# Kernel tuning notes

Hardware: AMD Instinct MI355X
Metric: run time of the kernel (lower is better)

Reference implementation:

```python
import jax, jax.numpy as jnp
import numpy as np

VOCAB = 32000
D_MODEL = 1024
PATCH_LEN = 16
NHEAD = 8
B = 8
S = 4096


def setup_inputs() -> dict:
    key = jax.random.key(0)
    ks = jax.random.split(key, 8)
    token_inputs = jax.random.randint(ks[0], (B, S), 0, VOCAB, dtype=jnp.int64 if jax.config.jax_enable_x64 else jnp.int32)
    attention_mask = jax.random.randint(ks[1], (B, S), 0, 2).astype(bool)
    emb_weight = jax.random.normal(ks[2], (VOCAB, D_MODEL), dtype=jnp.float32) * 0.02
    patch_query = jax.random.normal(ks[3], (1, 1, D_MODEL), dtype=jnp.float32) * 0.02
    # nn.MultiheadAttention packed in-projection [3D, D] and out projection [D, D]
    lim = 1.0 / np.sqrt(D_MODEL)
    in_proj_w = jax.random.uniform(ks[4], (3 * D_MODEL, D_MODEL), jnp.float32, -lim, lim)
    in_proj_b = jnp.zeros((3 * D_MODEL,), jnp.float32)
    out_w = jax.random.uniform(ks[5], (D_MODEL, D_MODEL), jnp.float32, -lim, lim)
    out_b = jnp.zeros((D_MODEL,), jnp.float32)
    return {
        "token_inputs": token_inputs,
        "attention_mask": attention_mask,
        "emb_weight": emb_weight,
        "patch_query": patch_query,
        "in_proj_w": in_proj_w,
        "in_proj_b": in_proj_b,
        "out_w": out_w,
        "out_b": out_b,
    }


def reference(token_inputs, attention_mask, emb_weight, patch_query, in_proj_w, in_proj_b, out_w, out_b):
    d_model = emb_weight.shape[1]
    h, dh = NHEAD, d_model // NHEAD
    L = PATCH_LEN

    tok_emb = emb_weight[token_inputs]              # [B, S, D]
    bsz, seqlen, _ = tok_emb.shape
    # seqlen chosen divisible by PATCH_LEN -> pad_len == 0 (matches torch path)
    num_patches = seqlen // L
    BP = bsz * num_patches
    patch_tokens = tok_emb.reshape(BP, L, d_model)  # [BP, L, D]
    patch_mask = attention_mask.reshape(BP, L)      # True = valid token

    patch_valid = patch_mask.any(axis=1)            # [BP]
    # force position 0 valid for fully-empty patches (safe softmax)
    safe_mask = patch_mask | ((~patch_valid)[:, None] & (jnp.arange(L) == 0)[None, :])

    wq, wk, wv = jnp.split(in_proj_w, 3, axis=0)    # each [D, D]
    bq, bk, bv = jnp.split(in_proj_b, 3, axis=0)

    q = patch_query[0, 0] @ wq.T + bq               # [D] (same query for all patches)
    k = patch_tokens @ wk.T + bk                    # [BP, L, D]
    v = patch_tokens @ wv.T + bv                    # [BP, L, D]

    qh = q.reshape(h, dh)                           # [H, dh]
    kh = k.reshape(BP, L, h, dh)                    # [BP, L, H, dh]
    vh = v.reshape(BP, L, h, dh)

    scale = 1.0 / jnp.sqrt(jnp.asarray(dh, q.dtype))
    scores = jnp.einsum('hd,blhd->bhl', qh, kh) * scale   # [BP, H, L]
    scores = jnp.where(safe_mask[:, None, :], scores, -jnp.inf)
    attn = jax.nn.softmax(scores, axis=-1)                # [BP, H, L]

    ctx = jnp.einsum('bhl,blhd->bhd', attn, vh).reshape(BP, d_model)
    patch_latent = ctx @ out_w.T + out_b                  # [BP, D]

    patch_latent = patch_latent.reshape(bsz, num_patches, d_model)
    pv = patch_valid.reshape(bsz, num_patches)
    patch_latent = patch_latent * pv[..., None].astype(patch_latent.dtype)
    return patch_latent, pv
```

## Files before the change

kernel.cpp:

```cpp
#include <hip/hip_runtime.h>
#include <stdint.h>

typedef unsigned short u16;

#define OUT_LATENT (2048*1024)
#define SCALE 0.08838834764831845f

typedef float f32x4v __attribute__((ext_vector_type(4)));
typedef short s16x8  __attribute__((ext_vector_type(8)));

static __device__ inline u16 f2bf(float f) {
    union { float f; uint32_t u; } v; v.f = f;
    uint32_t u = v.u;
    return (u16)((u + 0x7FFFu + ((u >> 16) & 1u)) >> 16);
}
static __device__ inline float bflo(uint32_t u) {
    union { uint32_t u; float f; } v; v.u = u << 16; return v.f;
}
static __device__ inline float bfhi(uint32_t u) {
    union { uint32_t u; float f; } v; v.u = u & 0xFFFF0000u; return v.f;
}
static __device__ __forceinline__ void async16(const u16* g, u16* l) {
    __builtin_amdgcn_global_load_lds(
        (const __attribute__((address_space(1))) void*)g,
        (__attribute__((address_space(3))) void*)l, 16, 0, 0);
}

__global__ __launch_bounds__(256) void k_prep(
    const float* __restrict__ ipw, const float* __restrict__ ipb,
    const float* __restrict__ pq, const float* __restrict__ ow,
    u16* __restrict__ wv_dst, u16* __restrict__ ow_dst,
    u16* __restrict__ qkb, float* __restrict__ sb) {
    __shared__ float qs[128];
    __shared__ float part[128];
    int t = threadIdx.x, b = blockIdx.x;

    if (b < 2048) {
        const float* src; u16* dst; int idx;
        if (b < 1024) { src = ipw + (size_t)2048 * 1024; dst = wv_dst; idx = b * 1024 + t * 4; }
        else          { src = ow;                        dst = ow_dst; idx = (b - 1024) * 1024 + t * 4; }
        float4 f = *(const float4*)(src + idx);
        ushort4 o; o.x = f2bf(f.x); o.y = f2bf(f.y); o.z = f2bf(f.z); o.w = f2bf(f.w);
        *(ushort4*)(dst + idx) = o;
        return;
    }

    int bb = b - 2048;
    int h = bb >> 3, jseg = bb & 7;
    {
        int dl = t >> 1, half = t & 1;
        const float* wrow = ipw + (size_t)(h * 128 + dl) * 1024 + half * 512;
        const float* pqh = pq + half * 512;
        float a = 0.f;
        #pragma unroll 8
        for (int j = 0; j < 512; j += 4) {
            float4 w = *(const float4*)(wrow + j);
            float4 p = *(const float4*)(pqh + j);
            a = fmaf(w.x, p.x, a); a = fmaf(w.y, p.y, a);
            a = fmaf(w.z, p.z, a); a = fmaf(w.w, p.w, a);
        }
        a += __shfl_xor(a, 1);
        if (!half) qs[dl] = a + ipb[h * 128 + dl];
    }
    __syncthreads();
    int jl = t & 127, dh = t >> 7;
    float acc = 0.f;
    const float* wbase = ipw + (size_t)(1024 + h * 128 + dh * 64) * 1024 + jseg * 128 + jl;
    #pragma unroll 8
    for (int d = 0; d < 64; ++d)
        acc = fmaf(qs[dh * 64 + d], wbase[(size_t)d * 1024], acc);
    if (dh) part[jl] = acc;
    __syncthreads();
    if (!dh) qkb[h * 1024 + jseg * 128 + jl] = f2bf((acc + part[jl]) * SCALE);
    if (jseg == 0 && t < 64) {
        const float* bk = ipb + 1024 + h * 128;
        float p = qs[t] * bk[t] + qs[t + 64] * bk[t + 64];
        #pragma unroll
        for (int m = 32; m >= 1; m >>= 1) p += __shfl_xor(p, m);
        if (t == 0) sb[h] = p * SCALE;
    }
}

__global__ __launch_bounds__(256) void k_attn(
    const int* __restrict__ tok_ids, const int* __restrict__ amask,
    const float* __restrict__ emb, const u16* __restrict__ qkb,
    const float* __restrict__ sb, u16* __restrict__ Mout,
    float* __restrict__ pv) {
    __shared__ u16 tokL[16][1032];
    __shared__ float scoresP[4][16][8];
    __shared__ float attnL[16][8];
    __shared__ int allzL;

    int bp = blockIdx.x, t = threadIdx.x;
    int wave = t >> 6, lane = t & 63, lrow = lane & 15, quad = lane >> 4;

    if (t < 16) {
        int any = (amask[bp * 16 + t] != 0);
        any |= __shfl_xor(any, 1); any |= __shfl_xor(any, 2);
        any |= __shfl_xor(any, 4); any |= __shfl_xor(any, 8);
        if (t == 0) { pv[bp] = any ? 1.f : 0.f; allzL = any ? 0 : 1; }
    }

    int row = t >> 4, c = t & 15;
    int tid = tok_ids[bp * 16 + row];
    const float* erow = emb + (size_t)tid * 1024;
    float4 ld[8];
    #pragma unroll
    for (int i = 0; i < 8; ++i) ld[i] = *(const float4*)(erow + (c + i * 16) * 4);

    s16x8 bfr[8];
    {
        const u16* qbase = qkb + (lane & 7) * 1024 + wave * 256 + quad * 8;
        #pragma unroll
        for (int s = 0; s < 8; ++s) bfr[s] = *(const s16x8*)(qbase + s * 32);
    }
    #pragma unroll
    for (int i = 0; i < 8; ++i) {
        ushort4 o; o.x = f2bf(ld[i].x); o.y = f2bf(ld[i].y);
        o.z = f2bf(ld[i].z); o.w = f2bf(ld[i].w);
        *(ushort4*)(&tokL[row][(c + i * 16) * 4]) = o;
    }
    #pragma unroll
    for (int i = 0; i < 8; ++i) ld[i] = *(const float4*)(erow + (c + (i + 8) * 16) * 4);
    #pragma unroll
    for (int i = 0; i < 8; ++i) {
        ushort4 o; o.x = f2bf(ld[i].x); o.y = f2bf(ld[i].y);
        o.z = f2bf(ld[i].z); o.w = f2bf(ld[i].w);
        *(ushort4*)(&tokL[row][(c + (i + 8) * 16) * 4]) = o;
    }
    __syncthreads();

    {
        f32x4v acc = (f32x4v){0.f, 0.f, 0.f, 0.f};
        const u16* arow = &tokL[lrow][wave * 256 + quad * 8];
        #pragma unroll
        for (int s = 0; s < 8; ++s) {
            s16x8 af = *(const s16x8*)(arow + s * 32);
            acc = __builtin_amdgcn_mfma_f32_16x16x32_bf16(af, bfr[s], acc, 0, 0, 0);
        }
        if (lrow < 8) {
            #pragma unroll
            for (int r = 0; r < 4; ++r) scoresP[wave][quad * 4 + r][lrow] = acc[r];
        }
    }
    __syncthreads();

    if (t < 128) {
        int hh = t >> 4, ll = t & 15;
        float s = scoresP[0][ll][hh] + scoresP[1][ll][hh]
                + scoresP[2][ll][hh] + scoresP[3][ll][hh] + sb[hh];
        bool valid = (amask[bp * 16 + ll] != 0) || (allzL && ll == 0);
        s = valid ? s : -1e30f;
        float mx = s;
        mx = fmaxf(mx, __shfl_xor(mx, 1)); mx = fmaxf(mx, __shfl_xor(mx, 2));
        mx = fmaxf(mx, __shfl_xor(mx, 4)); mx = fmaxf(mx, __shfl_xor(mx, 8));
        float e = __expf(s - mx);
        float sum = e;
        sum += __shfl_xor(sum, 1); sum += __shfl_xor(sum, 2);
        sum += __shfl_xor(sum, 4); sum += __shfl_xor(sum, 8);
        attnL[ll][hh] = e / sum;
    }
    __syncthreads();

    float macc[8][4];
    #pragma unroll
    for (int h = 0; h < 8; ++h)
        #pragma unroll
        for (int cc = 0; cc < 4; ++cc) macc[h][cc] = 0.f;
    #pragma unroll
    for (int ll = 0; ll < 16; ++ll) {
        uint2 tv = *(const uint2*)(&tokL[ll][t * 4]);
        float t0 = bflo(tv.x), t1 = bfhi(tv.x), t2 = bflo(tv.y), t3 = bfhi(tv.y);
        float4 a0 = *(const float4*)(&attnL[ll][0]);
        float4 a1 = *(const float4*)(&attnL[ll][4]);
        macc[0][0] = fmaf(a0.x, t0, macc[0][0]); macc[0][1] = fmaf(a0.x, t1, macc[0][1]);
        macc[0][2] = fmaf(a0.x, t2, macc[0][2]); macc[0][3] = fmaf(a0.x, t3, macc[0][3]);
        macc[1][0] = fmaf(a0.y, t0, macc[1][0]); macc[1][1] = fmaf(a0.y, t1, macc[1][1]);
        macc[1][2] = fmaf(a0.y, t2, macc[1][2]); macc[1][3] = fmaf(a0.y, t3, macc[1][3]);
        macc[2][0] = fmaf(a0.z, t0, macc[2][0]); macc[2][1] = fmaf(a0.z, t1, macc[2][1]);
        macc[2][2] = fmaf(a0.z, t2, macc[2][2]); macc[2][3] = fmaf(a0.z, t3, macc[2][3]);
        macc[3][0] = fmaf(a0.w, t0, macc[3][0]); macc[3][1] = fmaf(a0.w, t1, macc[3][1]);
        macc[3][2] = fmaf(a0.w, t2, macc[3][2]); macc[3][3] = fmaf(a0.w, t3, macc[3][3]);
        macc[4][0] = fmaf(a1.x, t0, macc[4][0]); macc[4][1] = fmaf(a1.x, t1, macc[4][1]);
        macc[4][2] = fmaf(a1.x, t2, macc[4][2]); macc[4][3] = fmaf(a1.x, t3, macc[4][3]);
        macc[5][0] = fmaf(a1.y, t0, macc[5][0]); macc[5][1] = fmaf(a1.y, t1, macc[5][1]);
        macc[5][2] = fmaf(a1.y, t2, macc[5][2]); macc[5][3] = fmaf(a1.y, t3, macc[5][3]);
        macc[6][0] = fmaf(a1.z, t0, macc[6][0]); macc[6][1] = fmaf(a1.z, t1, macc[6][1]);
        macc[6][2] = fmaf(a1.z, t2, macc[6][2]); macc[6][3] = fmaf(a1.z, t3, macc[6][3]);
        macc[7][0] = fmaf(a1.w, t0, macc[7][0]); macc[7][1] = fmaf(a1.w, t1, macc[7][1]);
        macc[7][2] = fmaf(a1.w, t2, macc[7][2]); macc[7][3] = fmaf(a1.w, t3, macc[7][3]);
    }
    #pragma unroll
    for (int h = 0; h < 8; ++h) {
        ushort4 o;
        o.x = f2bf(macc[h][0]); o.y = f2bf(macc[h][1]);
        o.z = f2bf(macc[h][2]); o.w = f2bf(macc[h][3]);
        *(ushort4*)(Mout + ((size_t)(h * 2048 + bp)) * 1024 + t * 4) = o;
    }
}

__device__ __forceinline__ void gemm128_bk64(
    const u16* __restrict__ A, const u16* __restrict__ B,
    u16* As, u16* Bs, f32x4v acc[4][4]) {
    int t = threadIdx.x;
    int wave = t >> 6, lane = t & 63, lrow = lane & 15, quad = lane >> 4;
    int wm = wave & 1, wn = wave >> 1;
    int tr = t >> 3, tc7 = t & 7;
    #pragma unroll
    for (int mi = 0; mi < 4; ++mi)
        #pragma unroll
        for (int ni = 0; ni < 4; ++ni) acc[mi][ni] = (f32x4v){0.f, 0.f, 0.f, 0.f};
    for (int step = 0; step < 16; ++step) {
        int k0 = step * 64;
        __syncthreads();
        #pragma unroll
        for (int rb = 0; rb < 128; rb += 32) {
            int r = rb + tr;
            int gofs = (tc7 ^ (r & 7)) * 8;
            async16(A + (size_t)r * 1024 + k0 + gofs, As + rb * 64 + t * 8);
            async16(B + (size_t)r * 1024 + k0 + gofs, Bs + rb * 64 + t * 8);
        }
        __syncthreads();
        #pragma unroll
        for (int kk = 0; kk < 2; ++kk) {
            s16x8 af[4], bf[4];
            #pragma unroll
            for (int i = 0; i < 4; ++i) {
                int ra = wm * 64 + i * 16 + lrow;
                af[i] = *(const s16x8*)(As + ra * 64 + (((kk * 4 + quad) ^ (ra & 7)) * 8));
                int rb2 = wn * 64 + i * 16 + lrow;
                bf[i] = *(const s16x8*)(Bs + rb2 * 64 + (((kk * 4 + quad) ^ (rb2 & 7)) * 8));
            }
            #pragma unroll
            for (int mi = 0; mi < 4; ++mi)
                #pragma unroll
                for (int ni = 0; ni < 4; ++ni)
                    acc[mi][ni] = __builtin_amdgcn_mfma_f32_16x16x32_bf16(af[mi], bf[ni], acc[mi][ni], 0, 0, 0);
        }
    }
}

__global__ __launch_bounds__(256) void k_gemm_ctx(
    const u16* __restrict__ M, const u16* __restrict__ wv,
    const float* __restrict__ ipb, u16* __restrict__ ctx) {
    __shared__ u16 As[128 * 64], Bs[128 * 64];
    int mb = blockIdx.x, h = blockIdx.y;
    f32x4v acc[4][4];
    gemm128_bk64(M + ((size_t)h * 2048 + mb * 128) * 1024,
                 wv + (size_t)h * 128 * 1024, As, Bs, acc);
    int t = threadIdx.x, wave = t >> 6, lane = t & 63, lrow = lane & 15, quad = lane >> 4;
    int wm = wave & 1, wn = wave >> 1;
    #pragma unroll
    for (int ni = 0; ni < 4; ++ni) {
        int n_g = h * 128 + wn * 64 + ni * 16 + lrow;
        float bias = ipb[2048 + n_g];
        #pragma unroll
        for (int mi = 0; mi < 4; ++mi) {
            #pragma unroll
            for (int r = 0; r < 4; ++r) {
                int m_g = mb * 128 + wm * 64 + mi * 16 + quad * 4 + r;
                ctx[(size_t)m_g * 1024 + n_g] = f2bf(acc[mi][ni][r] + bias);
            }
        }
    }
}

__global__ __launch_bounds__(256) void k_gemm_out(
    const u16* __restrict__ ctx, const u16* __restrict__ ow,
    const float* __restrict__ outb, const float* __restrict__ pv,
    float* __restrict__ out) {
    __shared__ u16 As[128 * 64], Bs[128 * 64];
    int mb = blockIdx.x, nb = blockIdx.y;
    f32x4v acc[4][4];
    gemm128_bk64(ctx + (size_t)mb * 128 * 1024,
                 ow + (size_t)nb * 128 * 1024, As, Bs, acc);
    int t = threadIdx.x, wave = t >> 6, lane = t & 63, lrow = lane & 15, quad = lane >> 4;
    int wm = wave & 1, wn = wave >> 1;
    #pragma unroll
    for (int ni = 0; ni < 4; ++ni) {
        int n_g = nb * 128 + wn * 64 + ni * 16 + lrow;
        float bias = outb[n_g];
        #pragma unroll
        for (int mi = 0; mi < 4; ++mi) {
            #pragma unroll
            for (int r = 0; r < 4; ++r) {
                int m_g = mb * 128 + wm * 64 + mi * 16 + quad * 4 + r;
                out[(size_t)m_g * 1024 + n_g] = (acc[mi][ni][r] + bias) * pv[m_g];
            }
        }
    }
    if (nb == 0 && t < 128) out[OUT_LATENT + mb * 128 + t] = pv[mb * 128 + t];
}

extern "C" void kernel_launch(void* const* d_in, const int* in_sizes, int n_in,
                              void* d_out, int out_size, void* d_ws, size_t ws_size,
                              hipStream_t stream) {
    const int*   tok = (const int*)d_in[0];
    const int*   msk = (const int*)d_in[1];
    const float* emb = (const float*)d_in[2];
    const float* pq  = (const float*)d_in[3];
    const float* ipw = (const float*)d_in[4];
    const float* ipb = (const float*)d_in[5];
    const float* ow  = (const float*)d_in[6];
    const float* ob  = (const float*)d_in[7];
    float* out = (float*)d_out;
    char* ws = (char*)d_ws;

    float* sb_f  = (float*)(ws + 4096);
    float* pv_f  = (float*)(ws + 8192);
    u16*   qk_b  = (u16*)(ws + 16384);
    u16*   wv_b  = (u16*)(ws + 32768);
    u16*   ow_b  = (u16*)(ws + 32768 + 2097152);
    u16*   ctx_b = (u16*)(ws + 32768 + 2 * 2097152);
    u16*   M_b   = (u16*)(ws + 32768 + 2 * 2097152 + 4194304);

    k_prep<<<dim3(2112), dim3(256), 0, stream>>>(ipw, ipb, pq, ow, wv_b, ow_b, qk_b, sb_f);
    k_attn<<<dim3(2048), dim3(256), 0, stream>>>(tok, msk, emb, qk_b, sb_f, M_b, pv_f);
    k_gemm_ctx<<<dim3(16, 8), dim3(256), 0, stream>>>(M_b, wv_b, ipb, ctx_b);
    k_gemm_out<<<dim3(16, 8), dim3(256), 0, stream>>>(ctx_b, ow_b, ob, pv_f, out);
}
```

Measured before the change: 299.1 us.

## Stage fp32 embeddings via async LDS loads and shrink GEMM K-tile to 32

The attention kernel now gathers embedding rows straight into shared memory as fp32 using global_load_lds, and converts to bf16 only when building the MFMA operands. The PV pass reads the fp32 values directly. This removes the register round-trip and the early conversion, at the cost of doubling shared memory for the token tile. The shared GEMM mainloop changes from a BK=64 tile with XOR swizzle to a BK=32 unswizzled tile over 32 steps, which adds barriers and may bring back LDS bank conflicts.

```diff
diff --git a/kernel.cpp b/kernel.cpp
--- a/kernel.cpp
+++ b/kernel.cpp
@@ -14,13 +14,7 @@
     uint32_t u = v.u;
     return (u16)((u + 0x7FFFu + ((u >> 16) & 1u)) >> 16);
 }
-static __device__ inline float bflo(uint32_t u) {
-    union { uint32_t u; float f; } v; v.u = u << 16; return v.f;
-}
-static __device__ inline float bfhi(uint32_t u) {
-    union { uint32_t u; float f; } v; v.u = u & 0xFFFF0000u; return v.f;
-}
-static __device__ __forceinline__ void async16(const u16* g, u16* l) {
+static __device__ __forceinline__ void async16(const void* g, void* l) {
     __builtin_amdgcn_global_load_lds(
         (const __attribute__((address_space(1))) void*)g,
         (__attribute__((address_space(3))) void*)l, 16, 0, 0);
@@ -81,18 +75,21 @@
     }
 }
 
+#define TROW 1028
 __global__ __launch_bounds__(256) void k_attn(
     const int* __restrict__ tok_ids, const int* __restrict__ amask,
     const float* __restrict__ emb, const u16* __restrict__ qkb,
     const float* __restrict__ sb, u16* __restrict__ Mout,
     float* __restrict__ pv) {
-    __shared__ u16 tokL[16][1032];
+    __shared__ float tokF[16 * TROW];
     __shared__ float scoresP[4][16][8];
     __shared__ float attnL[16][8];
     __shared__ int allzL;
 
     int bp = blockIdx.x, t = threadIdx.x;
     int wave = t >> 6, lane = t & 63, lrow = lane & 15, quad = lane >> 4;
+
+    int tid16 = tok_ids[bp * 16 + (lane & 15)];
 
     if (t < 16) {
         int any = (amask[bp * 16 + t] != 0);
@@ -101,41 +98,35 @@
         if (t == 0) { pv[bp] = any ? 1.f : 0.f; allzL = any ? 0 : 1; }
     }
 
-    int row = t >> 4, c = t & 15;
-    int tid = tok_ids[bp * 16 + row];
-    const float* erow = emb + (size_t)tid * 1024;
-    float4 ld[8];
-    #pragma unroll
-    for (int i = 0; i < 8; ++i) ld[i] = *(const float4*)(erow + (c + i * 16) * 4);
-
     s16x8 bfr[8];
     {
         const u16* qbase = qkb + (lane & 7) * 1024 + wave * 256 + quad * 8;
         #pragma unroll
         for (int s = 0; s < 8; ++s) bfr[s] = *(const s16x8*)(qbase + s * 32);
     }
-    #pragma unroll
-    for (int i = 0; i < 8; ++i) {
-        ushort4 o; o.x = f2bf(ld[i].x); o.y = f2bf(ld[i].y);
-        o.z = f2bf(ld[i].z); o.w = f2bf(ld[i].w);
-        *(ushort4*)(&tokL[row][(c + i * 16) * 4]) = o;
-    }
-    #pragma unroll
-    for (int i = 0; i < 8; ++i) ld[i] = *(const float4*)(erow + (c + (i + 8) * 16) * 4);
-    #pragma unroll
-    for (int i = 0; i < 8; ++i) {
-        ushort4 o; o.x = f2bf(ld[i].x); o.y = f2bf(ld[i].y);
-        o.z = f2bf(ld[i].z); o.w = f2bf(ld[i].w);
-        *(ushort4*)(&tokL[row][(c + (i + 8) * 16) * 4]) = o;
+
+    #pragma unroll
+    for (int i = 0; i < 16; ++i) {
+        int chunk = wave * 16 + i;
+        int row = chunk >> 2, q = chunk & 3;
+        int stid = __shfl(tid16, row);
+        async16(emb + (size_t)stid * 1024 + q * 256 + lane * 4,
+                tokF + row * TROW + q * 256 + lane * 4);
     }
     __syncthreads();
 
     {
         f32x4v acc = (f32x4v){0.f, 0.f, 0.f, 0.f};
-        const u16* arow = &tokL[lrow][wave * 256 + quad * 8];
+        const float* arow = tokF + lrow * TROW + wave * 256 + quad * 8;
         #pragma unroll
         for (int s = 0; s < 8; ++s) {
-            s16x8 af = *(const s16x8*)(arow + s * 32);
+            float4 f0 = *(const float4*)(arow + s * 32);
+            float4 f1 = *(const float4*)(arow + s * 32 + 4);
+            s16x8 af;
+            af[0] = (short)f2bf(f0.x); af[1] = (short)f2bf(f0.y);
+            af[2] = (short)f2bf(f0.z); af[3] = (short)f2bf(f0.w);
+            af[4] = (short)f2bf(f1.x); af[5] = (short)f2bf(f1.y);
+            af[6] = (short)f2bf(f1.z); af[7] = (short)f2bf(f1.w);
             acc = __builtin_amdgcn_mfma_f32_16x16x32_bf16(af, bfr[s], acc, 0, 0, 0);
         }
         if (lrow < 8) {
@@ -169,8 +160,8 @@
         for (int cc = 0; cc < 4; ++cc) macc[h][cc] = 0.f;
     #pragma unroll
     for (int ll = 0; ll < 16; ++ll) {
-        uint2 tv = *(const uint2*)(&tokL[ll][t * 4]);
-        float t0 = bflo(tv.x), t1 = bfhi(tv.x), t2 = bflo(tv.y), t3 = bfhi(tv.y);
+        float4 tv = *(const float4*)(tokF + ll * TROW + t * 4);
+        float t0 = tv.x, t1 = tv.y, t2 = tv.z, t3 = tv.w;
         float4 a0 = *(const float4*)(&attnL[ll][0]);
         float4 a1 = *(const float4*)(&attnL[ll][4]);
         macc[0][0] = fmaf(a0.x, t0, macc[0][0]); macc[0][1] = fmaf(a0.x, t1, macc[0][1]);
@@ -199,55 +190,47 @@
     }
 }
 
-__device__ __forceinline__ void gemm128_bk64(
+__device__ __forceinline__ void gemm128_mainloop(
     const u16* __restrict__ A, const u16* __restrict__ B,
     u16* As, u16* Bs, f32x4v acc[4][4]) {
     int t = threadIdx.x;
     int wave = t >> 6, lane = t & 63, lrow = lane & 15, quad = lane >> 4;
     int wm = wave & 1, wn = wave >> 1;
-    int tr = t >> 3, tc7 = t & 7;
+    int srow = t >> 2, sseg = (t & 3) * 8;
     #pragma unroll
     for (int mi = 0; mi < 4; ++mi)
         #pragma unroll
         for (int ni = 0; ni < 4; ++ni) acc[mi][ni] = (f32x4v){0.f, 0.f, 0.f, 0.f};
-    for (int step = 0; step < 16; ++step) {
-        int k0 = step * 64;
+    for (int step = 0; step < 32; ++step) {
+        int k0 = step * 32;
         __syncthreads();
-        #pragma unroll
-        for (int rb = 0; rb < 128; rb += 32) {
-            int r = rb + tr;
-            int gofs = (tc7 ^ (r & 7)) * 8;
-            async16(A + (size_t)r * 1024 + k0 + gofs, As + rb * 64 + t * 8);
-            async16(B + (size_t)r * 1024 + k0 + gofs, Bs + rb * 64 + t * 8);
-        }
+        async16(A + (size_t)srow * 1024 + k0 + sseg,        As + t * 8);
+        async16(A + (size_t)(srow + 64) * 1024 + k0 + sseg, As + (256 + t) * 8);
+        async16(B + (size_t)srow * 1024 + k0 + sseg,        Bs + t * 8);
+        async16(B + (size_t)(srow + 64) * 1024 + k0 + sseg, Bs + (256 + t) * 8);
         __syncthreads();
-        #pragma unroll
-        for (int kk = 0; kk < 2; ++kk) {
-            s16x8 af[4], bf[4];
+        s16x8 af[4], bf[4];
+        #pragma unroll
+        for (int i = 0; i < 4; ++i) {
+            af[i] = *(const s16x8*)(As + (wm * 64 + i * 16 + lrow) * 32 + quad * 8);
+            bf[i] = *(const s16x8*)(Bs + (wn * 64 + i * 16 + lrow) * 32 + quad * 8);
+        }
+        #pragma unroll
+        for (int mi = 0; mi < 4; ++mi)
             #pragma unroll
-            for (int i = 0; i < 4; ++i) {
-                int ra = wm * 64 + i * 16 + lrow;
-                af[i] = *(const s16x8*)(As + ra * 64 + (((kk * 4 + quad) ^ (ra & 7)) * 8));
-                int rb2 = wn * 64 + i * 16 + lrow;
-                bf[i] = *(const s16x8*)(Bs + rb2 * 64 + (((kk * 4 + quad) ^ (rb2 & 7)) * 8));
-            }
-            #pragma unroll
-            for (int mi = 0; mi < 4; ++mi)
-                #pragma unroll
-                for (int ni = 0; ni < 4; ++ni)
-                    acc[mi][ni] = __builtin_amdgcn_mfma_f32_16x16x32_bf16(af[mi], bf[ni], acc[mi][ni], 0, 0, 0);
-        }
+            for (int ni = 0; ni < 4; ++ni)
+                acc[mi][ni] = __builtin_amdgcn_mfma_f32_16x16x32_bf16(af[mi], bf[ni], acc[mi][ni], 0, 0, 0);
     }
 }
 
 __global__ __launch_bounds__(256) void k_gemm_ctx(
     const u16* __restrict__ M, const u16* __restrict__ wv,
     const float* __restrict__ ipb, u16* __restrict__ ctx) {
-    __shared__ u16 As[128 * 64], Bs[128 * 64];
+    __shared__ u16 As[128 * 32], Bs[128 * 32];
     int mb = blockIdx.x, h = blockIdx.y;
     f32x4v acc[4][4];
-    gemm128_bk64(M + ((size_t)h * 2048 + mb * 128) * 1024,
-                 wv + (size_t)h * 128 * 1024, As, Bs, acc);
+    gemm128_mainloop(M + ((size_t)h * 2048 + mb * 128) * 1024,
+                     wv + (size_t)h * 128 * 1024, As, Bs, acc);
     int t = threadIdx.x, wave = t >> 6, lane = t & 63, lrow = lane & 15, quad = lane >> 4;
     int wm = wave & 1, wn = wave >> 1;
     #pragma unroll
@@ -269,11 +252,11 @@
     const u16* __restrict__ ctx, const u16* __restrict__ ow,
     const float* __restrict__ outb, const float* __restrict__ pv,
     float* __restrict__ out) {
-    __shared__ u16 As[128 * 64], Bs[128 * 64];
+    __shared__ u16 As[128 * 32], Bs[128 * 32];
     int mb = blockIdx.x, nb = blockIdx.y;
     f32x4v acc[4][4];
-    gemm128_bk64(ctx + (size_t)mb * 128 * 1024,
-                 ow + (size_t)nb * 128 * 1024, As, Bs, acc);
+    gemm128_mainloop(ctx + (size_t)mb * 128 * 1024,
+                     ow + (size_t)nb * 128 * 1024, As, Bs, acc);
     int t = threadIdx.x, wave = t >> 6, lane = t & 63, lrow = lane & 15, quad = lane >> 4;
     int wm = wave & 1, wn = wave >> 1;
     #pragma unroll
```

After: 303.5 us. About the same (+1.5%).
